# Optimization experiments

Hardware: AMD Instinct MI355X
Metric: run time of the kernel (lower is better)

The kernel has to match this reference:

```python
import jax, jax.numpy as jnp
import numpy as np

HEAD_DIM = 64
SCALE = HEAD_DIM ** (-0.5)


def setup_inputs() -> dict:
    key = jax.random.key(0)
    kq, kk, kv = jax.random.split(key, 3)
    B, H, S, D = 2, 12, 2048, HEAD_DIM
    query = jax.random.normal(kq, (B, H, S, D), dtype=jnp.float32)
    k = jax.random.normal(kk, (B, H, S, D), dtype=jnp.float32)
    v = jax.random.normal(kv, (B, H, S, D), dtype=jnp.float32)
    mask = jnp.ones((1, 1, S, S), dtype=jnp.int32)
    return {"query": query, "key": k, "value": v, "mask": mask}


def reference(query, key, value, mask):
    # scores: [B, H, S, S]
    scores = jnp.einsum("bhqd,bhkd->bhqk", query, key) * SCALE
    scores = jnp.where(mask == 0, -jnp.inf, scores)
    probs = jax.nn.softmax(scores, axis=-1)
    # dropout = 0.0 -> identity
    out = jnp.einsum("bhqk,bhkd->bhqd", probs, value)
    return out
```

## Files before the change

### kernel.cpp

```cpp
#include <hip/hip_runtime.h>

#define SDIM 2048
#define DDIM 64
#define QT   64
#define NT   32
#define NT2  64
#define SCL2  (0.125f * 1.4426950408889634f)

typedef __attribute__((ext_vector_type(8))) short          bf16x8;
typedef __attribute__((ext_vector_type(4))) short          bf16x4;
typedef __attribute__((ext_vector_type(8))) unsigned short ushort8;
typedef __attribute__((ext_vector_type(4))) unsigned short us4;
typedef __attribute__((ext_vector_type(4))) float          f32x4;

__device__ __forceinline__ unsigned short f2bf(float x) {
    unsigned int u = __float_as_uint(x);
    u += 0x7FFFu + ((u >> 16) & 1u);
    return (unsigned short)(u >> 16);
}

__device__ __forceinline__ f32x4 mfma16(bf16x4 a, bf16x4 b, f32x4 c) {
#if __has_builtin(__builtin_amdgcn_mfma_f32_16x16x16bf16_1k)
    return __builtin_amdgcn_mfma_f32_16x16x16bf16_1k(a, b, c, 0, 0, 0);
#else
    asm volatile("v_mfma_f32_16x16x16_bf16 %0, %1, %2, %0" : "+v"(c) : "v"(a), "v"(b));
    return c;
#endif
}

__device__ __forceinline__ void cp16(const void* g, void* l) {
    __builtin_amdgcn_global_load_lds(
        (__attribute__((address_space(1))) void*)(uintptr_t)g,
        (__attribute__((address_space(3))) void*)(unsigned int)(uintptr_t)l,
        16, 0, 0);
}

__global__ __launch_bounds__(256)
void prep_kv(const float* __restrict__ Kp, const float* __restrict__ Vp,
             unsigned short* __restrict__ wsK, unsigned short* __restrict__ wsV)
{
    __shared__ alignas(16) unsigned short vstage[64 * DDIM];
    const int tid = threadIdx.x;
    const int t   = blockIdx.x;
    const int bh  = blockIdx.y;
    const size_t tb   = ((size_t)bh * NT + t) * (64 * DDIM);
    const size_t gsrc = (size_t)bh * SDIM * DDIM + (size_t)t * 64 * DDIM;

    const int key = tid >> 2;
    const int d0  = (tid & 3) << 4;
    const int sw  = (key & 7) << 3;

    {
        const float* src = Kp + gsrc + key * DDIM + d0;
        float4 a0 = ((const float4*)src)[0];
        float4 a1 = ((const float4*)src)[1];
        float4 a2 = ((const float4*)src)[2];
        float4 a3 = ((const float4*)src)[3];
        ushort8 w0, w1;
        w0[0]=f2bf(a0.x); w0[1]=f2bf(a0.y); w0[2]=f2bf(a0.z); w0[3]=f2bf(a0.w);
        w0[4]=f2bf(a1.x); w0[5]=f2bf(a1.y); w0[6]=f2bf(a1.z); w0[7]=f2bf(a1.w);
        w1[0]=f2bf(a2.x); w1[1]=f2bf(a2.y); w1[2]=f2bf(a2.z); w1[3]=f2bf(a2.w);
        w1[4]=f2bf(a3.x); w1[5]=f2bf(a3.y); w1[6]=f2bf(a3.z); w1[7]=f2bf(a3.w);
        *(ushort8*)&wsK[tb + key * 64 + ( d0      ^ sw)] = w0;
        *(ushort8*)&wsK[tb + key * 64 + ((d0 + 8) ^ sw)] = w1;
    }
    {
        const float* src = Vp + gsrc + key * DDIM + d0;
        float4 a0 = ((const float4*)src)[0];
        float4 a1 = ((const float4*)src)[1];
        float4 a2 = ((const float4*)src)[2];
        float4 a3 = ((const float4*)src)[3];
        ushort8 w0, w1;
        w0[0]=f2bf(a0.x); w0[1]=f2bf(a0.y); w0[2]=f2bf(a0.z); w0[3]=f2bf(a0.w);
        w0[4]=f2bf(a1.x); w0[5]=f2bf(a1.y); w0[6]=f2bf(a1.z); w0[7]=f2bf(a1.w);
        w1[0]=f2bf(a2.x); w1[1]=f2bf(a2.y); w1[2]=f2bf(a2.z); w1[3]=f2bf(a2.w);
        w1[4]=f2bf(a3.x); w1[5]=f2bf(a3.y); w1[6]=f2bf(a3.z); w1[7]=f2bf(a3.w);
        *(ushort8*)&vstage[key * 64 + ( d0      ^ sw)] = w0;
        *(ushort8*)&vstage[key * 64 + ((d0 + 8) ^ sw)] = w1;
    }
    __syncthreads();
    {
        const int d   = tid >> 2;
        const int k0  = (tid & 3) << 4;
        const int s_  = k0 >> 5;
        const int k00 = k0 & 31;
        const int vm2 = (d >> 1) & 7;
        unsigned short vals[16];
        #pragma unroll
        for (int j = 0; j < 16; ++j) {
            const int k = k0 + j;
            vals[j] = vstage[k * 64 + (d ^ ((k & 7) << 3))];
        }
        const size_t vbase = tb + s_ * 2048 + d * 32;
        #pragma unroll
        for (int j = 0; j < 4; ++j) {
            const int c = (k00 >> 2) + j;
            us4 o = { vals[4*j], vals[4*j+1], vals[4*j+2], vals[4*j+3] };
            *(us4*)&wsV[vbase + ((c ^ vm2) << 2)] = o;
        }
    }
}

__global__ __launch_bounds__(512)
void attn64_main(const float* __restrict__ Qp,
                 const unsigned short* __restrict__ wsK,
                 const unsigned short* __restrict__ wsV,
                 float* __restrict__ Op)
{
    __shared__ alignas(16) unsigned short kbuf[4][2048];
    __shared__ alignas(16) unsigned short vbuf[4][2048];

    const int tid  = threadIdx.x;
    const int lane = tid & 63;
    const int w    = tid >> 6;
    const int qg   = w & 3;
    const int par  = w >> 2;
    const int lo4  = lane & 15;
    const int hi2  = lane >> 4;
    const int l7s  = (lo4 & 7) << 3;
    const int vm2  = (lo4 >> 1) & 7;

    const int qt = blockIdx.x;
    const int bh = blockIdx.y;

    const unsigned short* Kt = wsK + (size_t)bh * (SDIM * DDIM);
    const unsigned short* Vt = wsV + (size_t)bh * (SDIM * DDIM);

    const int chك = w & 3;
    const bool isK = (w < 4);
    const unsigned short* gbase = (isK ? Kt : Vt) + (chك << 9) + lane * 8;
    auto stage = [&](int t, int b) {
        unsigned short* l = (isK ? &kbuf[b][0] : &vbuf[b][0]) + (chك << 9) + lane * 8;
        cp16(gbase + ((size_t)t << 11), l);
    };

    stage(0, 0);
    stage(1, 1);

    bf16x8 qf[2];
    {
        const float* Qb = Qp + (size_t)bh * SDIM * DDIM;
        const int qrow = qt * QT + qg * 16 + lo4;
        #pragma unroll
        for (int ks = 0; ks < 2; ++ks) {
            const float* src = Qb + (size_t)qrow * DDIM + ks * 32 + hi2 * 8;
            float4 a = ((const float4*)src)[0];
            float4 b = ((const float4*)src)[1];
            bf16x8 tq;
            tq[0] = (short)f2bf(a.x * SCL2); tq[1] = (short)f2bf(a.y * SCL2);
            tq[2] = (short)f2bf(a.z * SCL2); tq[3] = (short)f2bf(a.w * SCL2);
            tq[4] = (short)f2bf(b.x * SCL2); tq[5] = (short)f2bf(b.y * SCL2);
            tq[6] = (short)f2bf(b.z * SCL2); tq[7] = (short)f2bf(b.w * SCL2);
            qf[ks] = tq;
        }
    }

    int kidx[2], vidx[2];
    #pragma unroll
    for (int ks = 0; ks < 2; ++ks) kidx[ks] = lo4 * 64 + ((ks * 32 + hi2 * 8) ^ l7s);
    #pragma unroll
    for (int n = 0; n < 2; ++n)   vidx[n]  = lo4 * 32 + (((4 * n + hi2) ^ vm2) << 2);

    const short ov = (lo4 == 0) ? (short)0x3F80 : (short)0;
    const bf16x4 af = { ov, ov, ov, ov };

    f32x4 oacc[4];
    f32x4 acc5 = f32x4{0.f, 0.f, 0.f, 0.f};
    #pragma unroll
    for (int n = 0; n < 4; ++n) oacc[n] = f32x4{0.f, 0.f, 0.f, 0.f};

    const unsigned short* kbR0 = &kbuf[par][0];
    const unsigned short* vbR0 = &vbuf[par][0];
    const unsigned short* kbR1 = &kbuf[2 + par][0];
    const unsigned short* vbR1 = &vbuf[2 + par][0];

    auto tilebody = [&](const unsigned short* kb, const unsigned short* vb) {
        f32x4 s[2];
        s[0] = f32x4{0.f, 0.f, 0.f, 0.f};
        s[1] = f32x4{0.f, 0.f, 0.f, 0.f};
        __builtin_amdgcn_s_setprio(1);
        #pragma unroll
        for (int ks = 0; ks < 2; ++ks) {
            #pragma unroll
            for (int n = 0; n < 2; ++n) {
                bf16x8 kf = *(const bf16x8*)&kb[kidx[ks] + n * 1024];
                s[n] = __builtin_amdgcn_mfma_f32_16x16x32_bf16(kf, qf[ks], s[n], 0, 0, 0);
            }
        }
        __builtin_amdgcn_s_setprio(0);
        bf16x4 pkk[2];
        #pragma unroll
        for (int n = 0; n < 2; ++n) {
            const float p0 = exp2f(s[n][0]);
            const float p1 = exp2f(s[n][1]);
            const float p2 = exp2f(s[n][2]);
            const float p3 = exp2f(s[n][3]);
            unsigned int lo, hi;
            asm("v_cvt_pk_bf16_f32 %0, %1, %2" : "=v"(lo) : "v"(p0), "v"(p1));
            asm("v_cvt_pk_bf16_f32 %0, %1, %2" : "=v"(hi) : "v"(p2), "v"(p3));
            union { unsigned int u[2]; bf16x4 v; } r;
            r.u[0] = lo; r.u[1] = hi;
            pkk[n] = r.v;
        }
        __builtin_amdgcn_s_setprio(1);
        #pragma unroll
        for (int n = 0; n < 2; ++n) {
            acc5 = mfma16(af, pkk[n], acc5);
            #pragma unroll
            for (int db = 0; db < 4; ++db) {
                bf16x4 vf = *(const bf16x4*)&vb[vidx[n] + db * 512];
                oacc[db] = mfma16(vf, pkk[n], oacc[db]);
            }
        }
        __builtin_amdgcn_s_setprio(0);
    };

    asm volatile("s_waitcnt vmcnt(0) lgkmcnt(0)" ::: "memory");
    __builtin_amdgcn_s_barrier();

    #pragma unroll 1
    for (int j = 0; j < 16; ++j) {
        stage(4 * j + 2, 2);
        stage(4 * j + 3, 3);
        tilebody(kbR0, vbR0);
        asm volatile("s_waitcnt vmcnt(0) lgkmcnt(0)" ::: "memory");
        __builtin_amdgcn_s_barrier();
        if (j < 15) {
            stage(4 * j + 4, 0);
            stage(4 * j + 5, 1);
        }
        tilebody(kbR1, vbR1);
        asm volatile("s_waitcnt vmcnt(0) lgkmcnt(0)" ::: "memory");
        __builtin_amdgcn_s_barrier();
    }

    __syncthreads();
    float* combO = (float*)&kbuf[0][0];
    float* combL = (float*)&vbuf[0][0];
    const int cb = qg * 64 + lane;
    if (par) {
        #pragma unroll
        for (int db = 0; db < 4; ++db)
            *(f32x4*)&combO[cb * 16 + db * 4] = oacc[db];
        *(f32x4*)&combL[cb * 4] = acc5;
    }
    __syncthreads();
    if (!par) {
        #pragma unroll
        for (int db = 0; db < 4; ++db)
            oacc[db] += *(const f32x4*)&combO[cb * 16 + db * 4];
        acc5 += *(const f32x4*)&combL[cb * 4];

        const float lsum = __shfl(acc5[0], lo4);
        const float inv = 1.f / lsum;
        const int q = qt * QT + qg * 16 + lo4;
        float* dst = Op + (size_t)bh * SDIM * DDIM + (size_t)q * DDIM;
        #pragma unroll
        for (int db = 0; db < 4; ++db) {
            float4 o = { oacc[db][0] * inv, oacc[db][1] * inv,
                         oacc[db][2] * inv, oacc[db][3] * inv };
            *(float4*)&dst[16 * db + hi2 * 4] = o;
        }
    }
}

__global__ __launch_bounds__(256)
void attn64_fallback(const float* __restrict__ Qp, const float* __restrict__ Kp,
                     const float* __restrict__ Vp, float* __restrict__ Op)
{
    __shared__ alignas(16) unsigned short kls[64 * DDIM];
    __shared__ alignas(16) unsigned short vls[DDIM * 64];
    __shared__ alignas(16) unsigned short pls[4][16 * 64];

    const int tid  = threadIdx.x;
    const int lane = tid & 63;
    const int wave = tid >> 6;
    const int lo4  = lane & 15;
    const int hi2  = lane >> 4;
    const int qt = blockIdx.x;
    const int bh = blockIdx.y;

    const size_t base = (size_t)bh * SDIM * DDIM;
    const float* Qb = Qp + base;
    const float* Kb = Kp + base;
    const float* Vb = Vp + base;
    float*       Ob = Op + base;

    bf16x8 qf[2];
    {
        const int qrow = qt * QT + wave * 16 + lo4;
        #pragma unroll
        for (int ks = 0; ks < 2; ++ks) {
            const float* src = Qb + (size_t)qrow * DDIM + ks * 32 + hi2 * 8;
            float4 a = ((const float4*)src)[0];
            float4 b = ((const float4*)src)[1];
            bf16x8 tq;
            tq[0] = (short)f2bf(a.x * SCL2); tq[1] = (short)f2bf(a.y * SCL2);
            tq[2] = (short)f2bf(a.z * SCL2); tq[3] = (short)f2bf(a.w * SCL2);
            tq[4] = (short)f2bf(b.x * SCL2); tq[5] = (short)f2bf(b.y * SCL2);
            tq[6] = (short)f2bf(b.z * SCL2); tq[7] = (short)f2bf(b.w * SCL2);
            qf[ks] = tq;
        }
    }

    float mrow[4], lrow[4];
    f32x4 oacc[4];
    #pragma unroll
    for (int r = 0; r < 4; ++r) { mrow[r] = -1e30f; lrow[r] = 0.f; }
    #pragma unroll
    for (int n = 0; n < 4; ++n) oacc[n] = f32x4{0.f, 0.f, 0.f, 0.f};

    for (int t0 = 0; t0 < SDIM; t0 += 64) {
        __syncthreads();
        {
            const int key = tid >> 2;
            const int d0  = (tid & 3) << 4;
            const float* src = Kb + (size_t)(t0 + key) * DDIM + d0;
            float4 a0 = ((const float4*)src)[0];
            float4 a1 = ((const float4*)src)[1];
            float4 a2 = ((const float4*)src)[2];
            float4 a3 = ((const float4*)src)[3];
            ushort8 w0, w1;
            w0[0]=f2bf(a0.x); w0[1]=f2bf(a0.y); w0[2]=f2bf(a0.z); w0[3]=f2bf(a0.w);
            w0[4]=f2bf(a1.x); w0[5]=f2bf(a1.y); w0[6]=f2bf(a1.z); w0[7]=f2bf(a1.w);
            w1[0]=f2bf(a2.x); w1[1]=f2bf(a2.y); w1[2]=f2bf(a2.z); w1[3]=f2bf(a2.w);
            w1[4]=f2bf(a3.x); w1[5]=f2bf(a3.y); w1[6]=f2bf(a3.z); w1[7]=f2bf(a3.w);
            const int sw = (key & 7) << 3;
            *(ushort8*)&kls[key * 64 + ( d0      ^ sw)] = w0;
            *(ushort8*)&kls[key * 64 + ((d0 + 8) ^ sw)] = w1;
        }
        {
            const int key = lane;
            const int d0  = wave << 4;
            const float* src = Vb + (size_t)(t0 + key) * DDIM + d0;
            float4 b0 = ((const float4*)src)[0];
            float4 b1 = ((const float4*)src)[1];
            float4 b2 = ((const float4*)src)[2];
            float4 b3 = ((const float4*)src)[3];
            float vv[16] = { b0.x,b0.y,b0.z,b0.w, b1.x,b1.y,b1.z,b1.w,
                             b2.x,b2.y,b2.z,b2.w, b3.x,b3.y,b3.z,b3.w };
            #pragma unroll
            for (int j = 0; j < 16; ++j) {
                const int d = d0 + j;
                vls[d * 64 + (key ^ ((d & 7) << 3))] = f2bf(vv[j]);
            }
        }
        __syncthreads();

        f32x4 s[4];
        #pragma unroll
        for (int n = 0; n < 4; ++n) s[n] = f32x4{0.f, 0.f, 0.f, 0.f};
        #pragma unroll
        for (int ks = 0; ks < 2; ++ks) {
            const int kb = ks * 32 + hi2 * 8;
            #pragma unroll
            for (int n = 0; n < 4; ++n) {
                const int key = lo4 + 16 * n;
                bf16x8 b = *(const bf16x8*)&kls[key * 64 + (kb ^ ((key & 7) << 3))];
                s[n] = __builtin_amdgcn_mfma_f32_16x16x32_bf16(qf[ks], b, s[n], 0, 0, 0);
            }
        }
        #pragma unroll
        for (int r = 0; r < 4; ++r) {
            float tmax = fmaxf(fmaxf(s[0][r], s[1][r]), fmaxf(s[2][r], s[3][r]));
            tmax = fmaxf(tmax, __shfl_xor(tmax, 1));
            tmax = fmaxf(tmax, __shfl_xor(tmax, 2));
            tmax = fmaxf(tmax, __shfl_xor(tmax, 4));
            tmax = fmaxf(tmax, __shfl_xor(tmax, 8));
            const float mn   = fmaxf(mrow[r], tmax);
            const float corr = exp2f(mrow[r] - mn);
            mrow[r] = mn;
            float rs = 0.f;
            #pragma unroll
            for (int n = 0; n < 4; ++n) {
                const float p = exp2f(s[n][r] - mn);
                s[n][r] = p;
                rs += p;
            }
            rs += __shfl_xor(rs, 1);
            rs += __shfl_xor(rs, 2);
            rs += __shfl_xor(rs, 4);
            rs += __shfl_xor(rs, 8);
            lrow[r] = lrow[r] * corr + rs;
            #pragma unroll
            for (int n = 0; n < 4; ++n) oacc[n][r] *= corr;
        }
        #pragma unroll
        for (int r = 0; r < 4; ++r) {
            const int q  = hi2 * 4 + r;
            const int sw = (q & 7) << 3;
            #pragma unroll
            for (int n = 0; n < 4; ++n)
                pls[wave][q * 64 + ((lo4 + 16 * n) ^ sw)] = f2bf(s[n][r]);
        }
        __syncthreads();
        #pragma unroll
        for (int ks = 0; ks < 2; ++ks) {
            const int kb = ks * 32 + hi2 * 8;
            bf16x8 a = *(const bf16x8*)&pls[wave][lo4 * 64 + (kb ^ ((lo4 & 7) << 3))];
            #pragma unroll
            for (int n = 0; n < 4; ++n) {
                const int d = 16 * n + lo4;
                bf16x8 b = *(const bf16x8*)&vls[d * 64 + (kb ^ ((d & 7) << 3))];
                oacc[n] = __builtin_amdgcn_mfma_f32_16x16x32_bf16(a, b, oacc[n], 0, 0, 0);
            }
        }
    }
    #pragma unroll
    for (int r = 0; r < 4; ++r) {
        const float inv = 1.f / lrow[r];
        const int q = qt * QT + wave * 16 + hi2 * 4 + r;
        float* dst = Ob + (size_t)q * DDIM;
        #pragma unroll
        for (int n = 0; n < 4; ++n)
            dst[16 * n + lo4] = oacc[n][r] * inv;
    }
}

extern "C" void kernel_launch(void* const* d_in, const int* in_sizes, int n_in,
                              void* d_out, int out_size, void* d_ws, size_t ws_size,
                              hipStream_t stream) {
    const float* Q = (const float*)d_in[0];
    const float* K = (const float*)d_in[1];
    const float* V = (const float*)d_in[2];
    float* O = (float*)d_out;
    const int BH = in_sizes[0] / (SDIM * DDIM);
    const size_t need = 2ull * BH * SDIM * DDIM * sizeof(unsigned short);

    if (ws_size >= need) {
        unsigned short* wsK = (unsigned short*)d_ws;
        unsigned short* wsV = wsK + (size_t)BH * SDIM * DDIM;
        prep_kv<<<dim3(NT, BH), dim3(256), 0, stream>>>(K, V, wsK, wsV);
        attn64_main<<<dim3(SDIM / QT, BH), dim3(512), 0, stream>>>(Q, wsK, wsV, O);
    } else {
        attn64_fallback<<<dim3(SDIM / QT, BH), dim3(256), 0, stream>>>(Q, K, V, O);
    }
}
```

Measured before the change: 57.56 us.

## Triple-buffer K/V tiles and remap blocks so each XCD shares heads

Expands the LDS staging from two to three tile-pair buffers so loads run two steps ahead, with a partial vmcnt wait instead of draining all outstanding loads each step. It also flattens the grid and remaps block indices so blocks placed round-robin on the 8 XCDs work on the same batch-heads, aiming for better L2 reuse of K/V. The cost is more LDS per block, which may lower occupancy, plus extra index arithmetic.

```diff
diff --git a/kernel.cpp b/kernel.cpp
--- a/kernel.cpp
+++ b/kernel.cpp
@@ -4,7 +4,6 @@
 #define DDIM 64
 #define QT   64
 #define NT   32
-#define NT2  64
 #define SCL2  (0.125f * 1.4426950408889634f)
 
 typedef __attribute__((ext_vector_type(8))) short          bf16x8;
@@ -105,10 +104,10 @@
 void attn64_main(const float* __restrict__ Qp,
                  const unsigned short* __restrict__ wsK,
                  const unsigned short* __restrict__ wsV,
-                 float* __restrict__ Op)
+                 float* __restrict__ Op, int bhpx)
 {
-    __shared__ alignas(16) unsigned short kbuf[4][2048];
-    __shared__ alignas(16) unsigned short vbuf[4][2048];
+    __shared__ alignas(16) unsigned short kbuf[6][2048];
+    __shared__ alignas(16) unsigned short vbuf[6][2048];
 
     const int tid  = threadIdx.x;
     const int lane = tid & 63;
@@ -120,22 +119,32 @@
     const int l7s  = (lo4 & 7) << 3;
     const int vm2  = (lo4 >> 1) & 7;
 
-    const int qt = blockIdx.x;
-    const int bh = blockIdx.y;
+    const int blk = blockIdx.x;
+    int bh, qt;
+    if (bhpx) {
+        const int loc = blk >> 3;
+        bh = (blk & 7) * bhpx + (loc >> 5);
+        qt = loc & 31;
+    } else {
+        bh = blk >> 5;
+        qt = blk & 31;
+    }
 
     const unsigned short* Kt = wsK + (size_t)bh * (SDIM * DDIM);
     const unsigned short* Vt = wsV + (size_t)bh * (SDIM * DDIM);
 
-    const int chك = w & 3;
+    const int chn = w & 3;
     const bool isK = (w < 4);
-    const unsigned short* gbase = (isK ? Kt : Vt) + (chك << 9) + lane * 8;
-    auto stage = [&](int t, int b) {
-        unsigned short* l = (isK ? &kbuf[b][0] : &vbuf[b][0]) + (chك << 9) + lane * 8;
-        cp16(gbase + ((size_t)t << 11), l);
-    };
-
-    stage(0, 0);
-    stage(1, 1);
+    const int off = (chn << 9) + lane * 8;
+    const unsigned short* gsrc0 = (isK ? Kt : Vt) + off;
+    unsigned short* const lK = &kbuf[0][0];
+    unsigned short* const lV = &vbuf[0][0];
+    unsigned short* const lmine = (isK ? lK : lV) + off;
+
+    cp16(gsrc0,        lmine);
+    cp16(gsrc0 + 2048, lmine + 2048);
+    cp16(gsrc0 + 4096, lmine + 4096);
+    cp16(gsrc0 + 6144, lmine + 6144);
 
     bf16x8 qf[2];
     {
@@ -169,10 +178,7 @@
     #pragma unroll
     for (int n = 0; n < 4; ++n) oacc[n] = f32x4{0.f, 0.f, 0.f, 0.f};
 
-    const unsigned short* kbR0 = &kbuf[par][0];
-    const unsigned short* vbR0 = &vbuf[par][0];
-    const unsigned short* kbR1 = &kbuf[2 + par][0];
-    const unsigned short* vbR1 = &vbuf[2 + par][0];
+    const int poff = par * 2048;
 
     auto tilebody = [&](const unsigned short* kb, const unsigned short* vb) {
         f32x4 s[2];
@@ -215,24 +221,31 @@
         __builtin_amdgcn_s_setprio(0);
     };
 
-    asm volatile("s_waitcnt vmcnt(0) lgkmcnt(0)" ::: "memory");
+    const unsigned short* gcur = gsrc0;
+
+    auto pairstep = [&](int SC, int SN, bool do_stage, bool last) {
+        if (do_stage) {
+            cp16(gcur + 8192,  (isK ? lK : lV) + SN * 2048 + off);
+            cp16(gcur + 10240, (isK ? lK : lV) + (SN + 1) * 2048 + off);
+        }
+        tilebody(lK + SC * 2048 + poff, lV + SC * 2048 + poff);
+        if (do_stage) { asm volatile("s_waitcnt vmcnt(2) lgkmcnt(0)" ::: "memory"); }
+        else          { asm volatile("s_waitcnt vmcnt(0) lgkmcnt(0)" ::: "memory"); }
+        if (!last) __builtin_amdgcn_s_barrier();
+        gcur += 4096;
+    };
+
+    asm volatile("s_waitcnt vmcnt(2) lgkmcnt(0)" ::: "memory");
     __builtin_amdgcn_s_barrier();
 
     #pragma unroll 1
-    for (int j = 0; j < 16; ++j) {
-        stage(4 * j + 2, 2);
-        stage(4 * j + 3, 3);
-        tilebody(kbR0, vbR0);
-        asm volatile("s_waitcnt vmcnt(0) lgkmcnt(0)" ::: "memory");
-        __builtin_amdgcn_s_barrier();
-        if (j < 15) {
-            stage(4 * j + 4, 0);
-            stage(4 * j + 5, 1);
-        }
-        tilebody(kbR1, vbR1);
-        asm volatile("s_waitcnt vmcnt(0) lgkmcnt(0)" ::: "memory");
-        __builtin_amdgcn_s_barrier();
-    }
+    for (int jj = 0; jj < 10; ++jj) {
+        pairstep(0, 4, true, false);
+        pairstep(2, 0, true, false);
+        pairstep(4, 2, true, false);
+    }
+    pairstep(0, 4, false, false);
+    pairstep(2, 0, false, true);
 
     __syncthreads();
     float* combO = (float*)&kbuf[0][0];
@@ -430,8 +443,9 @@
     if (ws_size >= need) {
         unsigned short* wsK = (unsigned short*)d_ws;
         unsigned short* wsV = wsK + (size_t)BH * SDIM * DDIM;
+        const int bhpx = (BH % 8 == 0) ? (BH / 8) : 0;
         prep_kv<<<dim3(NT, BH), dim3(256), 0, stream>>>(K, V, wsK, wsV);
-        attn64_main<<<dim3(SDIM / QT, BH), dim3(512), 0, stream>>>(Q, wsK, wsV, O);
+        attn64_main<<<dim3(BH * 32), dim3(512), 0, stream>>>(Q, wsK, wsV, O, bhpx);
     } else {
         attn64_fallback<<<dim3(SDIM / QT, BH), dim3(256), 0, stream>>>(Q, K, V, O);
     }
```

After: 57.43 us. No clear change (-0.2%).
